# Optimization experiments

Hardware: AMD Instinct MI355X
Metric: run time of the kernel (lower is better)

The kernel has to match this reference:

```python
import jax, jax.numpy as jnp
import numpy as np

LAGS = (1, 5, 10, 21, 30)
TOP_K = 8
LN_EPS = 1e-5


def setup_inputs() -> dict:
    key = jax.random.key(0)
    ks = jax.random.split(key, 12)
    B, N, T, H = 4, 64, 256, 256
    s = 1.0 / np.sqrt(H)
    return {
        'target_h': jax.random.normal(ks[0], (B, T, H), jnp.float32),
        'peer_h': jax.random.normal(ks[1], (B, N, T, H), jnp.float32),
        'peer_mask': jax.random.uniform(ks[2], (B, N)) > 0.1,
        'wq': jax.random.normal(ks[3], (H, H), jnp.float32) * s,
        'bq': jnp.zeros((H,), jnp.float32),
        'wk': jax.random.normal(ks[4], (H, H), jnp.float32) * s,
        'bk': jnp.zeros((H,), jnp.float32),
        'wv': jax.random.normal(ks[5], (H, H), jnp.float32) * s,
        'bv': jnp.zeros((H,), jnp.float32),
        'w1': jax.random.normal(ks[6], (H, H), jnp.float32) * s,
        'b1': jnp.zeros((H,), jnp.float32),
        'w2': jax.random.normal(ks[7], (H, H), jnp.float32) * s,
        'b2': jnp.zeros((H,), jnp.float32),
        'gamma': jnp.ones((H,), jnp.float32),
        'beta': jnp.zeros((H,), jnp.float32),
    }


def reference(target_h, peer_h, peer_mask, wq, bq, wk, bk, wv, bv,
              w1, b1, w2, b2, gamma, beta):
    B, N, T, H = peer_h.shape
    L = len(LAGS)
    lag = jnp.array(LAGS)
    # lag gather: t_idx[l, t] = t - lag[l]
    t_idx = jnp.arange(T)[None, :] - lag[:, None]            # [L, T]
    valid_time = t_idx >= 0                                  # [L, T]
    t_idx_c = jnp.maximum(t_idx, 0)
    phl = jnp.take(peer_h, t_idx_c, axis=2)                  # [B, N, L, T, H]
    phl = jnp.transpose(phl, (0, 3, 1, 2, 4))                # [B, T, N, L, H]

    Q = target_h @ wq.T + bq                                 # [B, T, H]
    K = phl @ wk.T + bk                                      # [B, T, N, L, H]
    V = phl @ wv.T + bv                                      # [B, T, N, L, H]

    logits = jnp.einsum('bth,btnlh->btnl', Q, K) / jnp.sqrt(jnp.float32(H))
    mask = valid_time.T[None, :, None, :] & peer_mask[:, None, :, None]
    logits = jnp.where(mask, logits, -jnp.inf)               # [B, T, N, L]

    NL = N * L
    k = min(TOP_K, NL)
    lf = logits.reshape(B, T, NL)
    _, topk_idx = jax.lax.top_k(lf, k)                       # [B, T, k]
    topk_vals = jnp.take_along_axis(lf, topk_idx, axis=-1)
    is_inf = jnp.isinf(topk_vals)
    all_inf = jnp.all(is_inf, axis=-1, keepdims=True)
    topk_safe = jnp.where(is_inf, -1e9, topk_vals)
    weights = jax.nn.softmax(topk_safe, axis=-1)
    weights = weights * (~all_inf).astype(weights.dtype)     # [B, T, k]

    V_flat = V.reshape(B, T, NL, H)
    V_sel = jnp.take_along_axis(V_flat, topk_idx[..., None], axis=2)  # [B, T, k, H]
    cs_y = jnp.einsum('btk,btkh->bth', weights, V_sel)       # [B, T, H]

    ffn = jax.nn.elu(cs_y @ w1.T + b1) @ w2.T + b2
    y = cs_y + ffn
    mu = jnp.mean(y, axis=-1, keepdims=True)
    var = jnp.var(y, axis=-1, keepdims=True)
    return (y - mu) / jnp.sqrt(var + LN_EPS) * gamma + beta
```

## Files before the change

kernel.cpp:

```cpp
#include <hip/hip_runtime.h>

#define H 256
#define B 4
#define N 64
#define T 256
#define L 5
#define TOPK 8

typedef __attribute__((ext_vector_type(8))) short bf16x8;
typedef __attribute__((ext_vector_type(4))) float f32x4;

__device__ __forceinline__ float wave_reduce_sum(float v) {
    #pragma unroll
    for (int off = 32; off > 0; off >>= 1) v += __shfl_xor(v, off, 64);
    return v;
}

__device__ __forceinline__ unsigned short f2bf(float x) {
    unsigned u = __float_as_uint(x);
    return (unsigned short)((u + 0x7fffu + ((u >> 16) & 1u)) >> 16);
}
__device__ __forceinline__ float bf2f(unsigned short h) {
    return __uint_as_float(((unsigned)h) << 16);
}

__global__ __launch_bounds__(256) void prep_kernel(
    const float* __restrict__ wq, const float* __restrict__ wk,
    const float* __restrict__ wv, const float* __restrict__ w1,
    const float* __restrict__ w2, const unsigned char* __restrict__ mask_raw,
    bf16x8* __restrict__ fragQ, bf16x8* __restrict__ fragK,
    bf16x8* __restrict__ fragV, bf16x8* __restrict__ frag1,
    bf16x8* __restrict__ frag2, int* __restrict__ maskI) {
    int bi = blockIdx.x;
    int tid = threadIdx.x;
    if (bi < 80) {
        int id = bi >> 4, tile = bi & 15;
        const float* src = (id == 0) ? wq : (id == 1) ? wk : (id == 2) ? wv
                          : (id == 3) ? w1 : w2;
        bf16x8* dst = (id == 0) ? fragQ : (id == 1) ? fragK : (id == 2) ? fragV
                     : (id == 3) ? frag1 : frag2;
        int splits = (id < 2) ? 3 : 2;
        int lane = tid & 63;
        __shared__ float Lt[256][20];
        if (id == 1) {
            int c4 = (tid & 3) * 4;
            for (int rr = 0; rr < 256; rr += 64) {
                int r = rr + (tid >> 2);
                *(float4*)&Lt[r][c4] = *(const float4*)(wk + (size_t)r * H + tile * 16 + c4);
            }
            __syncthreads();
        }
        for (int kk = 0; kk < 2; kk++) {
            int kstep = (tid >> 6) + kk * 4;
            int kbase = kstep * 32 + ((lane >> 4) * 8);
            float x[8];
            if (id == 1) {
                #pragma unroll
                for (int e = 0; e < 8; e++) x[e] = Lt[kbase + e][lane & 15];
            } else {
                int j = tile * 16 + (lane & 15);
                float4 v0 = *(const float4*)(src + (size_t)j * H + kbase);
                float4 v1 = *(const float4*)(src + (size_t)j * H + kbase + 4);
                x[0] = v0.x; x[1] = v0.y; x[2] = v0.z; x[3] = v0.w;
                x[4] = v1.x; x[5] = v1.y; x[6] = v1.z; x[7] = v1.w;
            }
            bf16x8 fh, fm, fl;
            #pragma unroll
            for (int e = 0; e < 8; e++) {
                unsigned short h = f2bf(x[e]);
                float r1 = x[e] - bf2f(h);
                unsigned short m = f2bf(r1);
                fh[e] = (short)h; fm[e] = (short)m;
                if (splits == 3) fl[e] = (short)f2bf(r1 - bf2f(m));
            }
            size_t base = ((size_t)(tile * 8 + kstep)) * 64 + lane;
            dst[base] = fh;
            dst[base + 8192] = fm;
            if (splits == 3) dst[base + 16384] = fl;
        }
        return;
    }
    __shared__ int nzOff, byteBad, intBad;
    if (tid == 0) { nzOff = 0; byteBad = 0; intBad = 0; }
    __syncthreads();
    unsigned char c = mask_raw[tid];
    if ((tid & 3) && c) atomicOr(&nzOff, 1);
    if (c > 1) atomicOr(&byteBad, 1);
    if (tid < 64) {
        unsigned int iv = ((const unsigned int*)mask_raw)[tid];
        if (iv > 1u) atomicOr(&intBad, 1);
    }
    __syncthreads();
    int v;
    if (nzOff && !byteBad)  v = (mask_raw[tid] != 0);
    else if (!intBad)       v = (((const unsigned int*)mask_raw)[tid] != 0);
    else                    v = (((const float*)mask_raw)[tid] != 0.0f);
    maskI[tid] = v;
}

template <int SPLITS, int EPI>
__global__ __launch_bounds__(256) void gemm_mfma_kernel(
    const float* __restrict__ A, const bf16x8* __restrict__ Wfrag,
    const float* __restrict__ bias, const float* __restrict__ rowscale,
    const float* __restrict__ resid, const float* __restrict__ gamma,
    const float* __restrict__ beta, float* __restrict__ C) {
    int m0 = blockIdx.x * 16;
    int tid = threadIdx.x, lane = tid & 63, w = tid >> 6;
    f32x4 acc[4] = {};
    const float* Abase = A + (size_t)(m0 + (lane & 15)) * H + ((lane >> 4) * 8);
    #pragma unroll 2
    for (int ks = 0; ks < 8; ks++) {
        float4 a0 = *(const float4*)(Abase + ks * 32);
        float4 a1 = *(const float4*)(Abase + ks * 32 + 4);
        float x[8] = {a0.x, a0.y, a0.z, a0.w, a1.x, a1.y, a1.z, a1.w};
        bf16x8 ah, am, al;
        #pragma unroll
        for (int e = 0; e < 8; e++) {
            unsigned short h = f2bf(x[e]);
            float r1 = x[e] - bf2f(h);
            unsigned short m = f2bf(r1);
            ah[e] = (short)h; am[e] = (short)m;
            if (SPLITS == 3) al[e] = (short)f2bf(r1 - bf2f(m));
        }
        bf16x8 bh[4], bm[4], bl[4];
        #pragma unroll
        for (int c = 0; c < 4; c++) {
            size_t base = ((size_t)((w * 4 + c) * 8 + ks)) * 64 + lane;
            bh[c] = Wfrag[base];
            bm[c] = Wfrag[base + 8192];
            if (SPLITS == 3) bl[c] = Wfrag[base + 16384];
        }
        #pragma unroll
        for (int c = 0; c < 4; c++) {
            acc[c] = __builtin_amdgcn_mfma_f32_16x16x32_bf16(ah, bh[c], acc[c], 0, 0, 0);
            acc[c] = __builtin_amdgcn_mfma_f32_16x16x32_bf16(ah, bm[c], acc[c], 0, 0, 0);
            acc[c] = __builtin_amdgcn_mfma_f32_16x16x32_bf16(am, bh[c], acc[c], 0, 0, 0);
            if (SPLITS == 3) {
                acc[c] = __builtin_amdgcn_mfma_f32_16x16x32_bf16(ah, bl[c], acc[c], 0, 0, 0);
                acc[c] = __builtin_amdgcn_mfma_f32_16x16x32_bf16(al, bh[c], acc[c], 0, 0, 0);
                acc[c] = __builtin_amdgcn_mfma_f32_16x16x32_bf16(am, bm[c], acc[c], 0, 0, 0);
            }
        }
    }
    __shared__ float Cl[16][260];
    int rbase = (lane >> 4) * 4;
    #pragma unroll
    for (int c = 0; c < 4; c++) {
        int col = (w * 4 + c) * 16 + (lane & 15);
        #pragma unroll
        for (int r = 0; r < 4; r++) Cl[rbase + r][col] = acc[c][r];
    }
    __syncthreads();
    int r = tid >> 4, cg = tid & 15;
    int m = m0 + r;
    float y[16];
    #pragma unroll
    for (int u = 0; u < 4; u++) {
        float4 v = *(float4*)&Cl[r][cg * 16 + u * 4];
        y[u * 4 + 0] = v.x; y[u * 4 + 1] = v.y; y[u * 4 + 2] = v.z; y[u * 4 + 3] = v.w;
    }
    if (EPI == 0) {
        #pragma unroll
        for (int j = 0; j < 16; j++) y[j] = (y[j] + bias[cg * 16 + j]) * 0.0625f;
    } else if (EPI == 2) {
        float bs = rowscale[m];
        #pragma unroll
        for (int j = 0; j < 16; j++) y[j] += bs * bias[cg * 16 + j];
    } else if (EPI == 3) {
        #pragma unroll
        for (int j = 0; j < 16; j++) {
            float x = y[j] + bias[cg * 16 + j];
            y[j] = (x > 0.0f) ? x : expm1f(x);
        }
    } else if (EPI == 4) {
        #pragma unroll
        for (int j = 0; j < 16; j++)
            y[j] += bias[cg * 16 + j] + resid[(size_t)m * H + cg * 16 + j];
        float s = 0.0f;
        #pragma unroll
        for (int j = 0; j < 16; j++) s += y[j];
        #pragma unroll
        for (int off = 1; off < 16; off <<= 1) s += __shfl_xor(s, off, 64);
        float mu = s * (1.0f / H);
        float sq = 0.0f;
        #pragma unroll
        for (int j = 0; j < 16; j++) { float d = y[j] - mu; sq += d * d; }
        #pragma unroll
        for (int off = 1; off < 16; off <<= 1) sq += __shfl_xor(sq, off, 64);
        float inv = rsqrtf(sq * (1.0f / H) + 1e-5f);
        #pragma unroll
        for (int j = 0; j < 16; j++)
            y[j] = (y[j] - mu) * inv * gamma[cg * 16 + j] + beta[cg * 16 + j];
    }
    #pragma unroll
    for (int u = 0; u < 4; u++) {
        float4 o = {y[u * 4], y[u * 4 + 1], y[u * 4 + 2], y[u * 4 + 3]};
        *(float4*)&C[(size_t)m * H + cg * 16 + u * 4] = o;
    }
}

__global__ __launch_bounds__(256) void logits_kernel(
    const float* __restrict__ Qk, const float* __restrict__ peer_h,
    const int* __restrict__ maskI, float* __restrict__ logits) {
    const int lags[L] = {1, 5, 10, 21, 30};
    int bi = blockIdx.x;
    int sec = bi & 7;
    int n = (bi >> 3) & 63;
    int b = bi >> 9;
    int tid = threadIdx.x, wave = tid >> 6, lane = tid & 63;
    int r0 = sec * 32;
    if (sec == 0) {
        const int cum[6] = {0, 1, 6, 16, 37, 67};
        if (tid < 67) {
            int l = 0;
            while (tid >= cum[l + 1]) l++;
            int t = tid - cum[l];
            logits[((size_t)(b * T + t)) * (N * L) + n * L + l] = -__builtin_inff();
        }
    }
    if (!maskI[b * N + n]) {
        if (tid < 32 * L) {
            int tl = tid / 5, l = tid - tl * 5;
            int t = r0 + tl + lags[l];
            if (t < T) logits[((size_t)(b * T + t)) * (N * L) + n * L + l] = -__builtin_inff();
        }
        return;
    }
    __shared__ float part[8][164];
    const float* prow = peer_h + ((size_t)(b * N + n) * T + r0) * H;
    const float* qb = Qk + (size_t)b * T * H;
    #pragma unroll 2
    for (int i = 0; i < 8; i++) {
        int tl = wave * 8 + i;
        float4 p = *(const float4*)(prow + (size_t)tl * H + 4 * lane);
        int tb = r0 + tl;
        float4 q[5];
        #pragma unroll
        for (int l = 0; l < L; l++) {
            int t = tb + lags[l];
            t = (t < T) ? t : (T - 1);
            q[l] = *(const float4*)(qb + (size_t)t * H + 4 * lane);
        }
        #pragma unroll
        for (int l = 0; l < L; l++) {
            float s = fmaf(p.x, q[l].x, fmaf(p.y, q[l].y, fmaf(p.z, q[l].z, p.w * q[l].w)));
            s += __shfl_xor(s, 1, 64);
            s += __shfl_xor(s, 2, 64);
            s += __shfl_xor(s, 4, 64);
            if ((lane & 7) == 0) part[lane >> 3][tl * 5 + l] = s;
        }
    }
    __syncthreads();
    if (tid < 32 * L) {
        int tl = tid / 5, l = tid - tl * 5;
        int t = r0 + tl + lags[l];
        if (t < T) {
            float s = 0.0f;
            #pragma unroll
            for (int g = 0; g < 8; g++) s += part[g][tid];
            logits[((size_t)(b * T + t)) * (N * L) + n * L + l] = s;
        }
    }
}

__global__ __launch_bounds__(256) void topk_gather_kernel(
    const float* __restrict__ logits, const float* __restrict__ peer_h,
    float* __restrict__ u, float* __restrict__ sw) {
    const int lags[L] = {1, 5, 10, 21, 30};
    int row = blockIdx.x;
    int b = row >> 8, t = row & 255;
    int tid = threadIdx.x;
    __shared__ float wS[TOPK];
    __shared__ int idxS[TOPK];
    __shared__ float swS;
    if (tid < 64) {
        int lane = tid;
        const float* lrow = logits + (size_t)row * (N * L);
        float v[5];
        #pragma unroll
        for (int i = 0; i < 5; i++) v[i] = lrow[lane + 64 * i];
        float tv[TOPK]; int tix[TOPK];
        for (int k = 0; k < TOPK; k++) {
            float bv = v[0]; int bidx = lane;
            #pragma unroll
            for (int i = 1; i < 5; i++) {
                if (v[i] > bv) { bv = v[i]; bidx = lane + 64 * i; }
            }
            #pragma unroll
            for (int off = 32; off > 0; off >>= 1) {
                float ov = __shfl_xor(bv, off, 64);
                int   oi = __shfl_xor(bidx, off, 64);
                if (ov > bv || (ov == bv && oi < bidx)) { bv = ov; bidx = oi; }
            }
            tv[k] = bv; tix[k] = bidx;
            if ((bidx & 63) == lane) v[bidx >> 6] = -__builtin_inff();
        }
        if (lane == 0) {
            float m = -__builtin_inff();
            for (int k = 0; k < TOPK; k++)
                if (tv[k] > -__builtin_inff()) m = fmaxf(m, tv[k]);
            float den = 0.0f, w[TOPK];
            for (int k = 0; k < TOPK; k++) {
                w[k] = (tv[k] > -__builtin_inff()) ? expf(tv[k] - m) : 0.0f;
                den += w[k];
            }
            float inv = (den > 0.0f) ? 1.0f / den : 0.0f;
            for (int k = 0; k < TOPK; k++) { wS[k] = w[k] * inv; idxS[k] = tix[k]; }
            swS = (den > 0.0f) ? 1.0f : 0.0f;
        }
    }
    __syncthreads();
    float acc = 0.0f;
    #pragma unroll
    for (int k = 0; k < TOPK; k++) {
        float w = wS[k];
        if (w > 0.0f) {
            int idx = idxS[k];
            int n = idx / L, l = idx % L;
            int tp = t - lags[l];
            acc += w * peer_h[(((size_t)(b * N + n)) * T + tp) * H + tid];
        }
    }
    u[(size_t)row * H + tid] = acc;
    if (tid == 0) sw[row] = swS;
}

extern "C" void kernel_launch(void* const* d_in, const int* in_sizes, int n_in,
                              void* d_out, int out_size, void* d_ws, size_t ws_size,
                              hipStream_t stream) {
    const float* target_h = (const float*)d_in[0];
    const float* peer_h   = (const float*)d_in[1];
    const unsigned char* peer_mask = (const unsigned char*)d_in[2];
    const float* wq = (const float*)d_in[3];
    const float* bq = (const float*)d_in[4];
    const float* wk = (const float*)d_in[5];
    const float* wv = (const float*)d_in[7];
    const float* bv = (const float*)d_in[8];
    const float* w1 = (const float*)d_in[9];
    const float* b1 = (const float*)d_in[10];
    const float* w2 = (const float*)d_in[11];
    const float* b2 = (const float*)d_in[12];
    const float* gamma = (const float*)d_in[13];
    const float* beta  = (const float*)d_in[14];
    float* out = (float*)d_out;

    char* ws = (char*)d_ws;
    size_t off = 0;
    auto wsa = [&](size_t bytes) -> void* {
        void* p = ws + off;
        off += (bytes + 255) & ~(size_t)255;
        return p;
    };
    int*    maskI  = (int*)wsa(B * N * sizeof(int));
    bf16x8* fragQ  = (bf16x8*)wsa(3 * 8192 * 16);
    bf16x8* fragK  = (bf16x8*)wsa(3 * 8192 * 16);
    bf16x8* fragV  = (bf16x8*)wsa(2 * 8192 * 16);
    bf16x8* frag1  = (bf16x8*)wsa(2 * 8192 * 16);
    bf16x8* frag2  = (bf16x8*)wsa(2 * 8192 * 16);
    float*  tmp    = (float*)wsa((size_t)B * T * H * 4);
    float*  Qk     = (float*)wsa((size_t)B * T * H * 4);
    float*  logits = (float*)wsa((size_t)B * T * N * L * 4);
    float*  u      = (float*)wsa((size_t)B * T * H * 4);
    float*  sw     = (float*)wsa((size_t)B * T * 4);
    float*  csy    = (float*)wsa((size_t)B * T * H * 4);
    float*  h1     = (float*)wsa((size_t)B * T * H * 4);

    prep_kernel<<<81, 256, 0, stream>>>(wq, wk, wv, w1, w2, peer_mask,
                                        fragQ, fragK, fragV, frag1, frag2, maskI);
    gemm_mfma_kernel<3, 0><<<B * T / 16, 256, 0, stream>>>(
        target_h, fragQ, bq, nullptr, nullptr, nullptr, nullptr, tmp);
    gemm_mfma_kernel<3, 1><<<B * T / 16, 256, 0, stream>>>(
        tmp, fragK, nullptr, nullptr, nullptr, nullptr, nullptr, Qk);
    logits_kernel<<<B * N * 8, 256, 0, stream>>>(Qk, peer_h, maskI, logits);
    topk_gather_kernel<<<B * T, 256, 0, stream>>>(logits, peer_h, u, sw);
    gemm_mfma_kernel<2, 2><<<B * T / 16, 256, 0, stream>>>(
        u, fragV, bv, sw, nullptr, nullptr, nullptr, csy);
    gemm_mfma_kernel<2, 3><<<B * T / 16, 256, 0, stream>>>(
        csy, frag1, b1, nullptr, nullptr, nullptr, nullptr, h1);
    gemm_mfma_kernel<2, 4><<<B * T / 16, 256, 0, stream>>>(
        h1, frag2, b2, nullptr, csy, gamma, beta, out);
}
```

Baseline: 200.7 us.

## Fuse V projection, FFN and LayerNorm GEMMs into one tail kernel

Replaces three separate GEMM launches (V projection with row-scaled bias, FFN first layer with ELU, FFN second layer with residual and LayerNorm) with a single kernel that keeps each 16-row tile in shared memory and registers across all three stages. This removes two kernel launches and the global round-trips for the csy and h1 intermediates, and keeps the residual in registers. The tradeoff is more registers held per thread (the A fragments for all 8 k-steps plus the residual), which may lower occupancy. The grid is still only 64 blocks.

```diff
diff --git a/kernel.cpp b/kernel.cpp
--- a/kernel.cpp
+++ b/kernel.cpp
@@ -9,12 +9,6 @@
 
 typedef __attribute__((ext_vector_type(8))) short bf16x8;
 typedef __attribute__((ext_vector_type(4))) float f32x4;
-
-__device__ __forceinline__ float wave_reduce_sum(float v) {
-    #pragma unroll
-    for (int off = 32; off > 0; off >>= 1) v += __shfl_xor(v, off, 64);
-    return v;
-}
 
 __device__ __forceinline__ unsigned short f2bf(float x) {
     unsigned u = __float_as_uint(x);
@@ -101,9 +95,7 @@
 template <int SPLITS, int EPI>
 __global__ __launch_bounds__(256) void gemm_mfma_kernel(
     const float* __restrict__ A, const bf16x8* __restrict__ Wfrag,
-    const float* __restrict__ bias, const float* __restrict__ rowscale,
-    const float* __restrict__ resid, const float* __restrict__ gamma,
-    const float* __restrict__ beta, float* __restrict__ C) {
+    const float* __restrict__ bias, float* __restrict__ C) {
     int m0 = blockIdx.x * 16;
     int tid = threadIdx.x, lane = tid & 63, w = tid >> 6;
     f32x4 acc[4] = {};
@@ -162,35 +154,6 @@
     if (EPI == 0) {
         #pragma unroll
         for (int j = 0; j < 16; j++) y[j] = (y[j] + bias[cg * 16 + j]) * 0.0625f;
-    } else if (EPI == 2) {
-        float bs = rowscale[m];
-        #pragma unroll
-        for (int j = 0; j < 16; j++) y[j] += bs * bias[cg * 16 + j];
-    } else if (EPI == 3) {
-        #pragma unroll
-        for (int j = 0; j < 16; j++) {
-            float x = y[j] + bias[cg * 16 + j];
-            y[j] = (x > 0.0f) ? x : expm1f(x);
-        }
-    } else if (EPI == 4) {
-        #pragma unroll
-        for (int j = 0; j < 16; j++)
-            y[j] += bias[cg * 16 + j] + resid[(size_t)m * H + cg * 16 + j];
-        float s = 0.0f;
-        #pragma unroll
-        for (int j = 0; j < 16; j++) s += y[j];
-        #pragma unroll
-        for (int off = 1; off < 16; off <<= 1) s += __shfl_xor(s, off, 64);
-        float mu = s * (1.0f / H);
-        float sq = 0.0f;
-        #pragma unroll
-        for (int j = 0; j < 16; j++) { float d = y[j] - mu; sq += d * d; }
-        #pragma unroll
-        for (int off = 1; off < 16; off <<= 1) sq += __shfl_xor(sq, off, 64);
-        float inv = rsqrtf(sq * (1.0f / H) + 1e-5f);
-        #pragma unroll
-        for (int j = 0; j < 16; j++)
-            y[j] = (y[j] - mu) * inv * gamma[cg * 16 + j] + beta[cg * 16 + j];
     }
     #pragma unroll
     for (int u = 0; u < 4; u++) {
@@ -323,6 +286,129 @@
     }
     u[(size_t)row * H + tid] = acc;
     if (tid == 0) sw[row] = swS;
+}
+
+__device__ __forceinline__ void mfma_stage2(
+    const bf16x8 ah[8], const bf16x8 am[8], const bf16x8* __restrict__ Wf,
+    int lane, int w, f32x4 acc[4]) {
+    #pragma unroll 2
+    for (int ks = 0; ks < 8; ks++) {
+        #pragma unroll
+        for (int c = 0; c < 4; c++) {
+            size_t base = ((size_t)((w * 4 + c) * 8 + ks)) * 64 + lane;
+            bf16x8 bh = Wf[base];
+            bf16x8 bm = Wf[base + 8192];
+            acc[c] = __builtin_amdgcn_mfma_f32_16x16x32_bf16(ah[ks], bh, acc[c], 0, 0, 0);
+            acc[c] = __builtin_amdgcn_mfma_f32_16x16x32_bf16(ah[ks], bm, acc[c], 0, 0, 0);
+            acc[c] = __builtin_amdgcn_mfma_f32_16x16x32_bf16(am[ks], bh, acc[c], 0, 0, 0);
+        }
+    }
+}
+
+__global__ __launch_bounds__(256) void tail_fused_kernel(
+    const float* __restrict__ u, const bf16x8* __restrict__ fragV,
+    const bf16x8* __restrict__ frag1, const bf16x8* __restrict__ frag2,
+    const float* __restrict__ bv, const float* __restrict__ b1,
+    const float* __restrict__ b2, const float* __restrict__ sw,
+    const float* __restrict__ gamma, const float* __restrict__ beta,
+    float* __restrict__ out) {
+    int m0 = blockIdx.x * 16;
+    int tid = threadIdx.x, lane = tid & 63, w = tid >> 6;
+    int r = tid >> 4, cg = tid & 15;
+    __shared__ float Cl[16][260];
+    bf16x8 ah[8], am[8];
+    const float* Abase = u + (size_t)(m0 + (lane & 15)) * H + ((lane >> 4) * 8);
+    #pragma unroll
+    for (int ks = 0; ks < 8; ks++) {
+        float4 a0 = *(const float4*)(Abase + ks * 32);
+        float4 a1 = *(const float4*)(Abase + ks * 32 + 4);
+        float x[8] = {a0.x, a0.y, a0.z, a0.w, a1.x, a1.y, a1.z, a1.w};
+        #pragma unroll
+        for (int e = 0; e < 8; e++) {
+            unsigned short h = f2bf(x[e]);
+            ah[ks][e] = (short)h;
+            am[ks][e] = (short)f2bf(x[e] - bf2f(h));
+        }
+    }
+    float resid[16];
+    #pragma unroll 1
+    for (int stage = 0; stage < 3; stage++) {
+        f32x4 acc[4] = {};
+        mfma_stage2(ah, am, stage == 0 ? fragV : (stage == 1 ? frag1 : frag2),
+                    lane, w, acc);
+        int rbase = (lane >> 4) * 4;
+        __syncthreads();
+        #pragma unroll
+        for (int c = 0; c < 4; c++) {
+            int col = (w * 4 + c) * 16 + (lane & 15);
+            #pragma unroll
+            for (int rr = 0; rr < 4; rr++) Cl[rbase + rr][col] = acc[c][rr];
+        }
+        __syncthreads();
+        float y[16];
+        #pragma unroll
+        for (int uu = 0; uu < 4; uu++) {
+            float4 vv = *(float4*)&Cl[r][cg * 16 + uu * 4];
+            y[uu * 4 + 0] = vv.x; y[uu * 4 + 1] = vv.y;
+            y[uu * 4 + 2] = vv.z; y[uu * 4 + 3] = vv.w;
+        }
+        if (stage == 0) {
+            float bs = sw[m0 + r];
+            #pragma unroll
+            for (int j = 0; j < 16; j++) {
+                y[j] += bs * bv[cg * 16 + j];
+                resid[j] = y[j];
+            }
+        } else if (stage == 1) {
+            #pragma unroll
+            for (int j = 0; j < 16; j++) {
+                float x = y[j] + b1[cg * 16 + j];
+                y[j] = (x > 0.0f) ? x : expm1f(x);
+            }
+        } else {
+            #pragma unroll
+            for (int j = 0; j < 16; j++) y[j] += b2[cg * 16 + j] + resid[j];
+            float s = 0.0f;
+            #pragma unroll
+            for (int j = 0; j < 16; j++) s += y[j];
+            #pragma unroll
+            for (int off = 1; off < 16; off <<= 1) s += __shfl_xor(s, off, 64);
+            float mu = s * (1.0f / H);
+            float sq = 0.0f;
+            #pragma unroll
+            for (int j = 0; j < 16; j++) { float d = y[j] - mu; sq += d * d; }
+            #pragma unroll
+            for (int off = 1; off < 16; off <<= 1) sq += __shfl_xor(sq, off, 64);
+            float invs = rsqrtf(sq * (1.0f / H) + 1e-5f);
+            #pragma unroll
+            for (int j = 0; j < 16; j++)
+                y[j] = (y[j] - mu) * invs * gamma[cg * 16 + j] + beta[cg * 16 + j];
+            #pragma unroll
+            for (int uu = 0; uu < 4; uu++) {
+                float4 o = {y[uu * 4], y[uu * 4 + 1], y[uu * 4 + 2], y[uu * 4 + 3]};
+                *(float4*)&out[(size_t)(m0 + r) * H + cg * 16 + uu * 4] = o;
+            }
+            return;
+        }
+        #pragma unroll
+        for (int uu = 0; uu < 4; uu++) {
+            float4 o = {y[uu * 4], y[uu * 4 + 1], y[uu * 4 + 2], y[uu * 4 + 3]};
+            *(float4*)&Cl[r][cg * 16 + uu * 4] = o;
+        }
+        __syncthreads();
+        #pragma unroll
+        for (int ks = 0; ks < 8; ks++) {
+            float4 a0 = *(float4*)&Cl[lane & 15][ks * 32 + (lane >> 4) * 8];
+            float4 a1 = *(float4*)&Cl[lane & 15][ks * 32 + (lane >> 4) * 8 + 4];
+            float x[8] = {a0.x, a0.y, a0.z, a0.w, a1.x, a1.y, a1.z, a1.w};
+            #pragma unroll
+            for (int e = 0; e < 8; e++) {
+                unsigned short h = f2bf(x[e]);
+                ah[ks][e] = (short)h;
+                am[ks][e] = (short)f2bf(x[e] - bf2f(h));
+            }
+        }
+    }
 }
 
 extern "C" void kernel_launch(void* const* d_in, const int* in_sizes, int n_in,
@@ -362,21 +448,13 @@
     float*  logits = (float*)wsa((size_t)B * T * N * L * 4);
     float*  u      = (float*)wsa((size_t)B * T * H * 4);
     float*  sw     = (float*)wsa((size_t)B * T * 4);
-    float*  csy    = (float*)wsa((size_t)B * T * H * 4);
-    float*  h1     = (float*)wsa((size_t)B * T * H * 4);
 
     prep_kernel<<<81, 256, 0, stream>>>(wq, wk, wv, w1, w2, peer_mask,
                                         fragQ, fragK, fragV, frag1, frag2, maskI);
-    gemm_mfma_kernel<3, 0><<<B * T / 16, 256, 0, stream>>>(
-        target_h, fragQ, bq, nullptr, nullptr, nullptr, nullptr, tmp);
-    gemm_mfma_kernel<3, 1><<<B * T / 16, 256, 0, stream>>>(
-        tmp, fragK, nullptr, nullptr, nullptr, nullptr, nullptr, Qk);
+    gemm_mfma_kernel<3, 0><<<B * T / 16, 256, 0, stream>>>(target_h, fragQ, bq, tmp);
+    gemm_mfma_kernel<3, 1><<<B * T / 16, 256, 0, stream>>>(tmp, fragK, nullptr, Qk);
     logits_kernel<<<B * N * 8, 256, 0, stream>>>(Qk, peer_h, maskI, logits);
     topk_gather_kernel<<<B * T, 256, 0, stream>>>(logits, peer_h, u, sw);
-    gemm_mfma_kernel<2, 2><<<B * T / 16, 256, 0, stream>>>(
-        u, fragV, bv, sw, nullptr, nullptr, nullptr, csy);
-    gemm_mfma_kernel<2, 3><<<B * T / 16, 256, 0, stream>>>(
-        csy, frag1, b1, nullptr, nullptr, nullptr, nullptr, h1);
-    gemm_mfma_kernel<2, 4><<<B * T / 16, 256, 0, stream>>>(
-        h1, frag2, b2, nullptr, csy, gamma, beta, out);
-}
+    tail_fused_kernel<<<B * T / 16, 256, 0, stream>>>(u, fragV, frag1, frag2,
+                                                      bv, b1, b2, sw, gamma, beta, out);
+}
```

New measurement: 443.6 us. 2.21x slower.
